# Kernel tuning notes

Hardware: AMD Instinct MI355X
Metric: run time of the kernel (lower is better)

## Reference

```python
import jax, jax.numpy as jnp
import numpy as np

D_MODEL = 1024
N_HEADS = 16
D_HEAD = D_MODEL // N_HEADS


def setup_inputs() -> dict:
    key = jax.random.key(0)
    k1, k2, k3 = jax.random.split(key, 3)
    B, T = 2, 2048
    x = jax.random.normal(k1, (B, T, D_MODEL), dtype=jnp.float32)
    # kaiming_normal fan_out on torch Linear weight [out, in]: std = sqrt(2/out)
    qkv_w = jax.random.normal(k2, (3 * D_MODEL, D_MODEL), dtype=jnp.float32) * np.sqrt(2.0 / (3 * D_MODEL)).astype(np.float32)
    out_w = jax.random.normal(k3, (D_MODEL, D_MODEL), dtype=jnp.float32) * np.sqrt(2.0 / D_MODEL).astype(np.float32)
    return {"x": x, "qkv_w": qkv_w, "out_w": out_w}


def rotate_half(x):
    x1, x2 = x[..., : x.shape[-1] // 2], x[..., x.shape[-1] // 2 :]
    return jnp.concatenate((-x2, x1), axis=-1)


def reference(x, qkv_w, out_w):
    B, T, D = x.shape
    H, dh = N_HEADS, D_HEAD
    scale = dh ** -0.5

    qkv = jnp.einsum('btd,ed->bte', x, qkv_w)  # [B,T,3D]
    q, k, v = jnp.split(qkv, 3, axis=-1)
    # [B,H,T,dh]
    q = q.reshape(B, T, H, dh).transpose(0, 2, 1, 3)
    k = k.reshape(B, T, H, dh).transpose(0, 2, 1, 3)
    v = v.reshape(B, T, H, dh).transpose(0, 2, 1, 3)

    # rotary embeddings
    inv_freq = 1.0 / (10000.0 ** (jnp.arange(0, dh, 2, dtype=jnp.float32) / dh))
    t = jnp.arange(T, dtype=jnp.float32)
    freqs = jnp.einsum('i,j->ij', t, inv_freq)        # [T, dh/2]
    emb = jnp.concatenate((freqs, freqs), axis=-1)    # [T, dh]
    cos = jnp.cos(emb)[None, None]                    # [1,1,T,dh]
    sin = jnp.sin(emb)[None, None]
    q = q * cos + rotate_half(q) * sin
    k = k * cos + rotate_half(k) * sin

    scores = jnp.einsum('bhqd,bhkd->bhqk', q, k) * scale
    causal = jnp.tril(jnp.ones((T, T), dtype=bool))
    scores = jnp.where(causal, scores, -jnp.inf)
    attn = jax.nn.softmax(scores, axis=-1)
    out = jnp.einsum('bhqk,bhkd->bhqd', attn, v)      # [B,H,T,dh]
    out = out.transpose(0, 2, 1, 3).reshape(B, T, D)
    return jnp.einsum('btd,ed->bte', out, out_w)
```

## Files before the change

### kernel.cpp

```cpp
#include <hip/hip_runtime.h>
#include <hip/hip_bf16.h>
#include <cmath>

#define Bb   2
#define Tseq 2048
#define NH   16
#define DM   1024

using f32x4 = __attribute__((ext_vector_type(4))) float;
using s16x8 = __attribute__((ext_vector_type(8))) short;
using s16x4 = __attribute__((ext_vector_type(4))) short;

typedef const __attribute__((address_space(1))) unsigned char* as1p;
typedef __attribute__((address_space(3))) unsigned char* as3p;

static __device__ __forceinline__ void gload_lds16(const void* g, void* l){
  __builtin_amdgcn_global_load_lds((as1p)g, (as3p)l, 16, 0, 0);
}

#if defined(__has_builtin)
#if __has_builtin(__builtin_amdgcn_mfma_f32_16x16x16bf16_1k)
#define MFMA16(acc, va, pb) (acc) = __builtin_amdgcn_mfma_f32_16x16x16bf16_1k((va), (pb), (acc), 0, 0, 0)
#endif
#endif
#ifndef MFMA16
#define MFMA16(acc, va, pb) asm volatile("s_nop 1\n\tv_mfma_f32_16x16x16_bf16 %0, %1, %2, %0" : "+v"(acc) : "v"(va), "v"(pb))
#endif

static __device__ __forceinline__ float b2f(unsigned short u){
  union { unsigned int u; float f; } v; v.u = ((unsigned int)u) << 16; return v.f;
}
static __device__ __forceinline__ unsigned short f2b(float f){
  union { float f; unsigned int u; } v; v.f = f;
  unsigned int u = v.u;
  return (unsigned short)((u + 0x7fffu + ((u >> 16) & 1u)) >> 16);
}

__global__ void k_convert(const float* __restrict__ in, unsigned short* __restrict__ out, int n){
  int stride = gridDim.x * blockDim.x;
  for (int i = blockIdx.x * blockDim.x + threadIdx.x; i * 4 < n; i += stride) {
    const float4 v = *reinterpret_cast<const float4*>(in + (size_t)i * 4);
    ushort4 o; o.x = f2b(v.x); o.y = f2b(v.y); o.z = f2b(v.z); o.w = f2b(v.w);
    *reinterpret_cast<ushort4*>(out + (size_t)i * 4) = o;
  }
}

template<int MODE>
__global__ __launch_bounds__(256) void k_gemm_bt(const unsigned short* __restrict__ A,
                                                 const unsigned short* __restrict__ W,
                                                 void* __restrict__ Cout,
                                                 int M, int N, int K, int NYL,
                                                 unsigned short* __restrict__ qr,
                                                 unsigned short* __restrict__ kr){
  __shared__ unsigned short As[128*64];
  __shared__ unsigned short Bs[128*64];
  const int i = (int)blockIdx.x;
  const int xcd = i & 7, rr = i >> 3;
  const int bx = rr / NYL, by = xcd * NYL + (rr % NYL);
  const int bm = bx * 128, bn = by * 128;
  const int tid = threadIdx.x;
  const int lane = tid & 63, w = tid >> 6;
  const int wr = w >> 1, wc = w & 1;
  const int g = lane >> 4, ln = lane & 15;
  f32x4 acc[4][4] = {};
  char* asb = (char*)As + w * 4096;
  char* bsb = (char*)Bs + w * 4096;
  const int lrow8 = lane >> 3;
  const int kcolb = ((lane & 7) ^ lrow8) * 16;
  const size_t aro = (size_t)(bm + w * 32 + lrow8) * K;
  const size_t bro = (size_t)(bn + w * 32 + lrow8) * K;
  const int xr = (ln & 7) << 4;
  for (int k0 = 0; k0 < K; k0 += 64) {
    #pragma unroll
    for (int q4 = 0; q4 < 4; ++q4) {
      gload_lds16((const char*)(A + aro + (size_t)(q4 * 8) * K + k0) + kcolb, asb + q4 * 1024);
      gload_lds16((const char*)(W + bro + (size_t)(q4 * 8) * K + k0) + kcolb, bsb + q4 * 1024);
    }
    __syncthreads();
    #pragma unroll
    for (int kk = 0; kk < 2; ++kk) {
      s16x8 af[4], bfr[4];
      const int ro = (kk * 64 + g * 16) ^ xr;
      #pragma unroll
      for (int mt = 0; mt < 4; ++mt)
        af[mt] = *reinterpret_cast<const s16x8*>((char*)As + (wr*64 + mt*16 + ln) * 128 + ro);
      #pragma unroll
      for (int nt = 0; nt < 4; ++nt)
        bfr[nt] = *reinterpret_cast<const s16x8*>((char*)Bs + (wc*64 + nt*16 + ln) * 128 + ro);
      #pragma unroll
      for (int mt = 0; mt < 4; ++mt)
        #pragma unroll
        for (int nt = 0; nt < 4; ++nt)
          acc[mt][nt] = __builtin_amdgcn_mfma_f32_16x16x32_bf16(af[mt], bfr[nt], acc[mt][nt], 0, 0, 0);
    }
    __syncthreads();
  }
  if (MODE == 0) {
    #pragma unroll
    for (int mt = 0; mt < 4; ++mt)
      #pragma unroll
      for (int nt = 0; nt < 4; ++nt)
        #pragma unroll
        for (int r = 0; r < 4; ++r) {
          int row = bm + wr*64 + mt*16 + g*4 + r;
          int col = bn + wc*64 + nt*16 + ln;
          reinterpret_cast<float*>(Cout)[(size_t)row * N + col] = acc[mt][nt][r];
        }
  } else {
    const int region = bn >> 10;
    if (region == 2) {
      #pragma unroll
      for (int mt = 0; mt < 4; ++mt)
        #pragma unroll
        for (int nt = 0; nt < 4; ++nt)
          #pragma unroll
          for (int r = 0; r < 4; ++r) {
            int row = bm + wr*64 + mt*16 + g*4 + r;
            int col = bn + wc*64 + nt*16 + ln;
            reinterpret_cast<unsigned short*>(Cout)[(size_t)row * N + col] = f2b(acc[mt][nt][r]);
          }
    } else {
      const float if0 = exp2f(-(float)ln        * 0.4152410118074f);
      const float if1 = exp2f(-(float)(16 + ln) * 0.4152410118074f);
      const int h = ((bn + wc * 64) >> 6) & 15;
      unsigned short* dst = (region == 0) ? qr : kr;
      const float qs = (region == 0) ? 0.18033688011112042f : 1.0f;
      #pragma unroll
      for (int mt = 0; mt < 4; ++mt)
        #pragma unroll
        for (int r = 0; r < 4; ++r) {
          int row = bm + wr*64 + mt*16 + g*4 + r;
          int t = row & (Tseq - 1), b = row >> 11;
          float c0, s0, c1, s1;
          __sincosf((float)t * if0, &s0, &c0);
          __sincosf((float)t * if1, &s1, &c1);
          float v0 = (acc[mt][0][r] * c0 - acc[mt][2][r] * s0) * qs;
          float v1 = (acc[mt][1][r] * c1 - acc[mt][3][r] * s1) * qs;
          float v2 = (acc[mt][2][r] * c0 + acc[mt][0][r] * s0) * qs;
          float v3 = (acc[mt][3][r] * c1 + acc[mt][1][r] * s1) * qs;
          size_t base = ((size_t)(b * NH + h) * Tseq + t) * 64 + ln;
          dst[base]      = f2b(v0);
          dst[base + 16] = f2b(v1);
          dst[base + 32] = f2b(v2);
          dst[base + 48] = f2b(v3);
        }
    }
  }
}

__global__ __launch_bounds__(256) void k_vtrans(const unsigned short* __restrict__ qkv,
                                                unsigned short* __restrict__ vt){
  __shared__ unsigned short L[64*72];
  const int blk = blockIdx.x;
  const int tt64 = blk & 31, bh = blk >> 5;
  const int b = bh >> 4, h = bh & 15;
  const int t0 = tt64 * 64;
  const int tid = threadIdx.x;
  {
    const int tr = tid >> 2, c = tid & 3;
    const unsigned short* src = qkv + ((size_t)(b * Tseq) + t0 + tr) * 3072 + 2048 + h * 64 + c * 16;
    uint4 a0 = *reinterpret_cast<const uint4*>(src);
    uint4 a1 = *reinterpret_cast<const uint4*>(src + 8);
    *reinterpret_cast<uint4*>(&L[tr * 72 + c * 16])     = a0;
    *reinterpret_cast<uint4*>(&L[tr * 72 + c * 16 + 8]) = a1;
  }
  __syncthreads();
  {
    const int d = tid >> 2, c = tid & 3;
    unsigned int wq[8];
    #pragma unroll
    for (int j = 0; j < 8; ++j) {
      unsigned int lo = L[(c * 16 + 2 * j)     * 72 + d];
      unsigned int hi = L[(c * 16 + 2 * j + 1) * 72 + d];
      wq[j] = lo | (hi << 16);
    }
    unsigned short* dst = vt + ((size_t)bh * 64 + d) * Tseq + t0 + c * 16;
    *reinterpret_cast<uint4*>(dst)     = make_uint4(wq[0], wq[1], wq[2], wq[3]);
    *reinterpret_cast<uint4*>(dst + 8) = make_uint4(wq[4], wq[5], wq[6], wq[7]);
  }
}

__global__ __launch_bounds__(256, 2) void k_attn(const unsigned short* __restrict__ Qr,
                                                 const unsigned short* __restrict__ Kr,
                                                 const unsigned short* __restrict__ Vt,
                                                 unsigned short* __restrict__ Ao){
  __shared__ unsigned short Ks[2][64*64];
  __shared__ unsigned short Vs[2][64*64];
  __shared__ unsigned short Ps[4][16*72];
  const int i = (int)blockIdx.x;
  const int xcd = i & 7, r = i >> 3;
  const int bh = xcd * 4 + (r >> 4);
  const int pj = r & 15;
  const unsigned short* Q  = Qr + (size_t)bh * Tseq * 64;
  const unsigned short* Kp = Kr + (size_t)bh * Tseq * 64;
  const unsigned short* Vp = Vt + (size_t)bh * 64 * Tseq;
  const int tid = threadIdx.x;
  const int w = tid >> 6, lane = tid & 63;
  const int g = lane >> 4, ln = lane & 15;
  const int srow = tid >> 2;
  const int c2 = (tid & 3) * 2;
  const int scol = c2 * 8;
  const int swz = (srow & 7) << 4;
  const int wb0 = srow * 128 + ((c2 * 16)      ^ swz);
  const int wb1 = srow * 128 + ((c2 * 16 + 16) ^ swz);
  const int x0 = (g * 16)      ^ ((ln & 7) << 4);
  const int x1 = (64 + g * 16) ^ ((ln & 7) << 4);
  unsigned short* Pw = Ps[w];
  const int b = bh / NH, h = bh % NH;

  #pragma unroll
  for (int pass = 0; pass < 2; ++pass) {
    const int j = pass ? (31 - pj) : pj;
    const int q0 = j * 64;
    const int ntiles = j + 1;
    const int q0w = q0 + w * 16;

    s16x8 qf0 = *reinterpret_cast<const s16x8*>(&Q[(size_t)(q0w + ln) * 64 + g * 8]);
    s16x8 qf1 = *reinterpret_cast<const s16x8*>(&Q[(size_t)(q0w + ln) * 64 + 32 + g * 8]);

    f32x4 oacc[4] = {};
    float lsum = 0.f;

    {
      const unsigned short* gk = Kp + (size_t)srow * 64 + scol;
      const unsigned short* gv = Vp + (size_t)srow * Tseq + scol;
      uint4 k0 = *reinterpret_cast<const uint4*>(gk);
      uint4 k1 = *reinterpret_cast<const uint4*>(gk + 8);
      uint4 v0 = *reinterpret_cast<const uint4*>(gv);
      uint4 v1 = *reinterpret_cast<const uint4*>(gv + 8);
      *reinterpret_cast<uint4*>((char*)Ks[0] + wb0) = k0;
      *reinterpret_cast<uint4*>((char*)Ks[0] + wb1) = k1;
      *reinterpret_cast<uint4*>((char*)Vs[0] + wb0) = v0;
      *reinterpret_cast<uint4*>((char*)Vs[0] + wb1) = v1;
    }
    __syncthreads();
    int cur = 0;

    for (int kt = 0; kt < ntiles; ++kt) {
      const bool pre = (kt + 1 < ntiles);
      const int nxt = cur ^ 1;
      uint4 nk0, nk1, nv0, nv1;
      if (pre) {
        const unsigned short* gk = Kp + (size_t)((kt + 1) * 64 + srow) * 64 + scol;
        const unsigned short* gv = Vp + (size_t)srow * Tseq + (kt + 1) * 64 + scol;
        nk0 = *reinterpret_cast<const uint4*>(gk);
        nk1 = *reinterpret_cast<const uint4*>(gk + 8);
        nv0 = *reinterpret_cast<const uint4*>(gv);
        nv1 = *reinterpret_cast<const uint4*>(gv + 8);
      }
      f32x4 s[4] = {};
      const char* kb = (const char*)Ks[cur];
      __builtin_amdgcn_s_setprio(1);
      #pragma unroll
      for (int nt = 0; nt < 4; ++nt) {
        s16x8 kfa = *reinterpret_cast<const s16x8*>(kb + nt * 2048 + ln * 128 + x0);
        s16x8 kfb = *reinterpret_cast<const s16x8*>(kb + nt * 2048 + ln * 128 + x1);
        s[nt] = __builtin_amdgcn_mfma_f32_16x16x32_bf16(kfa, qf0, s[nt], 0, 0, 0);
        s[nt] = __builtin_amdgcn_mfma_f32_16x16x32_bf16(kfb, qf1, s[nt], 0, 0, 0);
      }
      __builtin_amdgcn_s_setprio(0);
      if (kt == ntiles - 1) {
        #pragma unroll
        for (int nt = 0; nt < 4; ++nt)
          #pragma unroll
          for (int r2 = 0; r2 < 4; ++r2)
            if (nt * 16 + g * 4 + r2 > w * 16 + ln) s[nt][r2] = -1e30f;
      }
      s16x4 pb[4];
      #pragma unroll
      for (int nt = 0; nt < 4; ++nt)
        #pragma unroll
        for (int r2 = 0; r2 < 4; ++r2) {
          float p = __builtin_amdgcn_exp2f(s[nt][r2]);
          lsum += p;
          pb[nt][r2] = (short)(__float_as_uint(p) >> 16);
        }
      const char* vb = (const char*)Vs[cur];
      __builtin_amdgcn_s_setprio(1);
      #pragma unroll
      for (int dt = 0; dt < 4; ++dt) {
        #pragma unroll
        for (int nt = 0; nt < 4; ++nt) {
          s16x4 va = *reinterpret_cast<const s16x4*>(vb + (dt * 16 + ln) * 128 + ((nt * 32 + g * 8) ^ ((ln & 7) << 4)));
          MFMA16(oacc[dt], va, pb[nt]);
        }
      }
      __builtin_amdgcn_s_setprio(0);
      if (pre) {
        *reinterpret_cast<uint4*>((char*)Ks[nxt] + wb0) = nk0;
        *reinterpret_cast<uint4*>((char*)Ks[nxt] + wb1) = nk1;
        *reinterpret_cast<uint4*>((char*)Vs[nxt] + wb0) = nv0;
        *reinterpret_cast<uint4*>((char*)Vs[nxt] + wb1) = nv1;
      }
      __syncthreads();
      cur ^= 1;
    }

    float l = lsum;
    l += __shfl_xor(l, 16);
    l += __shfl_xor(l, 32);
    float inv = 1.f / l;
    #pragma unroll
    for (int nt = 0; nt < 4; ++nt) {
      unsigned int lo = (unsigned int)f2b(oacc[nt][0] * inv) | ((unsigned int)f2b(oacc[nt][1] * inv) << 16);
      unsigned int hi = (unsigned int)f2b(oacc[nt][2] * inv) | ((unsigned int)f2b(oacc[nt][3] * inv) << 16);
      *reinterpret_cast<uint2*>(&Pw[ln * 72 + nt * 16 + g * 4]) = make_uint2(lo, hi);
    }
    asm volatile("s_waitcnt lgkmcnt(0)" ::: "memory");
    __builtin_amdgcn_sched_barrier(0);
    const int rr = lane >> 2;
    const int cc = (lane & 3) * 8;
    uint4 ov0 = *reinterpret_cast<const uint4*>(&Pw[rr * 72 + cc]);
    uint4 ov1 = *reinterpret_cast<const uint4*>(&Pw[rr * 72 + cc + 32]);
    int t = q0w + rr;
    unsigned short* orow = &Ao[((size_t)(b * Tseq + t) * DM) + h * 64];
    *reinterpret_cast<uint4*>(orow + cc)      = ov0;
    *reinterpret_cast<uint4*>(orow + cc + 32) = ov1;
  }
}

extern "C" void kernel_launch(void* const* d_in, const int* in_sizes, int n_in,
                              void* d_out, int out_size, void* d_ws, size_t ws_size,
                              hipStream_t stream) {
  const float* x    = (const float*)d_in[0];
  const float* qkvw = (const float*)d_in[1];
  const float* outw = (const float*)d_in[2];
  float* out = (float*)d_out;
  char* ws = (char*)d_ws;
  size_t off = 0;
  auto alloc = [&](size_t bytes)->void*{ void* p = ws + off; off += (bytes + 255) & ~(size_t)255; return p; };
  unsigned short* x_bf   = (unsigned short*)alloc((size_t)Bb*Tseq*DM*2);
  unsigned short* qw_bf  = (unsigned short*)alloc((size_t)3*DM*DM*2);
  unsigned short* ow_bf  = (unsigned short*)alloc((size_t)DM*DM*2);
  unsigned short* qkv_bf = (unsigned short*)alloc((size_t)Bb*Tseq*3*DM*2);
  unsigned short* qr     = (unsigned short*)alloc((size_t)Bb*NH*Tseq*64*2);
  unsigned short* kr     = (unsigned short*)alloc((size_t)Bb*NH*Tseq*64*2);
  unsigned short* vt     = (unsigned short*)alloc((size_t)Bb*NH*Tseq*64*2);
  unsigned short* ao     = (unsigned short*)alloc((size_t)Bb*Tseq*DM*2);
  (void)ws_size; (void)in_sizes; (void)n_in; (void)out_size;

  const int nx  = Bb*Tseq*DM;
  const int nqw = 3*DM*DM;
  const int now = DM*DM;
  k_convert<<<2048, 256, 0, stream>>>(x, x_bf, nx);
  k_convert<<<2048, 256, 0, stream>>>(qkvw, qw_bf, nqw);
  k_convert<<<1024, 256, 0, stream>>>(outw, ow_bf, now);
  k_gemm_bt<2><<<768, 256, 0, stream>>>(x_bf, qw_bf, qkv_bf, Bb*Tseq, 3*DM, DM, 3, qr, kr);
  k_vtrans<<<Bb*NH*(Tseq/64), 256, 0, stream>>>(qkv_bf, vt);
  k_attn<<<dim3(Bb*NH*16), 256, 0, stream>>>(qr, kr, vt, ao);
  k_gemm_bt<0><<<256, 256, 0, stream>>>(ao, ow_bf, out, Bb*Tseq, DM, DM, 1, qr, kr);
}
```

Before: 114.5 us.

## Fuse V transpose into QKV GEMM, merge converts, one query tile per attention block

Merges the three fp32-to-bf16 conversion launches into one kernel. The QKV GEMM now transposes the V tile through shared memory in its epilogue and writes Vt directly, which removes the intermediate qkv buffer and the separate transpose kernel. Attention now gives each block a single query tile, scheduled longest-first across twice as many blocks, and raises the occupancy hint from 2 to 5. The output staging reuses the K shared buffer, so the load balance across blocks changes and register pressure rises under the tighter launch bound.

Measured after the change: 123.7 us. +8.0%, slower.

```diff
diff --git a/kernel.cpp b/kernel.cpp
--- a/kernel.cpp
+++ b/kernel.cpp
@@ -36,12 +36,19 @@
   return (unsigned short)((u + 0x7fffu + ((u >> 16) & 1u)) >> 16);
 }
 
-__global__ void k_convert(const float* __restrict__ in, unsigned short* __restrict__ out, int n){
-  int stride = gridDim.x * blockDim.x;
-  for (int i = blockIdx.x * blockDim.x + threadIdx.x; i * 4 < n; i += stride) {
-    const float4 v = *reinterpret_cast<const float4*>(in + (size_t)i * 4);
+__global__ void k_convert3(const float* __restrict__ a, unsigned short* __restrict__ ab, int na,
+                           const float* __restrict__ b, unsigned short* __restrict__ bb, int nb,
+                           const float* __restrict__ c, unsigned short* __restrict__ cb, int nc){
+  const int q0 = na >> 2, q1 = nb >> 2, q2 = nc >> 2;
+  const int tot = q0 + q1 + q2;
+  const int stride = gridDim.x * blockDim.x;
+  for (int i = blockIdx.x * blockDim.x + threadIdx.x; i < tot; i += stride) {
+    const float* src; unsigned short* dst; int j = i;
+    if (j < q0) { src = a; dst = ab; }
+    else { j -= q0; if (j < q1) { src = b; dst = bb; } else { j -= q1; src = c; dst = cb; } }
+    float4 v = reinterpret_cast<const float4*>(src)[j];
     ushort4 o; o.x = f2b(v.x); o.y = f2b(v.y); o.z = f2b(v.z); o.w = f2b(v.w);
-    *reinterpret_cast<ushort4*>(out + (size_t)i * 4) = o;
+    reinterpret_cast<ushort4*>(dst)[j] = o;
   }
 }
 
@@ -51,7 +58,8 @@
                                                  void* __restrict__ Cout,
                                                  int M, int N, int K, int NYL,
                                                  unsigned short* __restrict__ qr,
-                                                 unsigned short* __restrict__ kr){
+                                                 unsigned short* __restrict__ kr,
+                                                 unsigned short* __restrict__ vt){
   __shared__ unsigned short As[128*64];
   __shared__ unsigned short Bs[128*64];
   const int i = (int)blockIdx.x;
@@ -109,16 +117,42 @@
   } else {
     const int region = bn >> 10;
     if (region == 2) {
-      #pragma unroll
-      for (int mt = 0; mt < 4; ++mt)
-        #pragma unroll
-        for (int nt = 0; nt < 4; ++nt)
-          #pragma unroll
-          for (int r = 0; r < 4; ++r) {
-            int row = bm + wr*64 + mt*16 + g*4 + r;
-            int col = bn + wc*64 + nt*16 + ln;
-            reinterpret_cast<unsigned short*>(Cout)[(size_t)row * N + col] = f2b(acc[mt][nt][r]);
-          }
+      unsigned short* tb = wc ? Bs : As;
+      #pragma unroll
+      for (int nt = 0; nt < 4; ++nt) {
+        const int lrow = nt * 16 + ln;
+        char* rowp = (char*)tb + lrow * 256;
+        const int sx = (lrow & 15) << 3;
+        #pragma unroll
+        for (int mt = 0; mt < 4; ++mt) {
+          const int t2 = (wr*64 + mt*16 + g*4) * 2;
+          unsigned int lo = (unsigned int)f2b(acc[mt][nt][0]) | ((unsigned int)f2b(acc[mt][nt][1]) << 16);
+          unsigned int hi = (unsigned int)f2b(acc[mt][nt][2]) | ((unsigned int)f2b(acc[mt][nt][3]) << 16);
+          *reinterpret_cast<uint2*>(rowp + (t2 ^ sx)) = make_uint2(lo, hi);
+        }
+      }
+      __syncthreads();
+      {
+        const int dcol = tid >> 1, half = tid & 1;
+        unsigned short* tb2 = (dcol < 64) ? As : Bs;
+        char* rowp = (char*)tb2 + (dcol & 63) * 256;
+        const int sx = (dcol & 15) << 3;
+        unsigned int buf[32];
+        #pragma unroll
+        for (int k = 0; k < 16; ++k) {
+          uint2 v = *reinterpret_cast<uint2*>(rowp + ((((half * 64 + k * 4) * 2) ^ sx)));
+          buf[k*2] = v.x; buf[k*2+1] = v.y;
+        }
+        const int h0 = (bn - 2048) >> 6;
+        const int hq = h0 + (dcol >> 6);
+        const int dd = dcol & 63;
+        const int row0 = bm + half * 64;
+        const int b = row0 >> 11, t0 = row0 & (Tseq - 1);
+        unsigned short* dst = vt + ((size_t)((b * NH + hq) * 64 + dd)) * Tseq + t0;
+        #pragma unroll
+        for (int k = 0; k < 8; ++k)
+          reinterpret_cast<uint4*>(dst)[k] = make_uint4(buf[k*4], buf[k*4+1], buf[k*4+2], buf[k*4+3]);
+      }
     } else {
       const float if0 = exp2f(-(float)ln        * 0.4152410118074f);
       const float if1 = exp2f(-(float)(16 + ln) * 0.4152410118074f);
@@ -148,49 +182,18 @@
   }
 }
 
-__global__ __launch_bounds__(256) void k_vtrans(const unsigned short* __restrict__ qkv,
-                                                unsigned short* __restrict__ vt){
-  __shared__ unsigned short L[64*72];
-  const int blk = blockIdx.x;
-  const int tt64 = blk & 31, bh = blk >> 5;
-  const int b = bh >> 4, h = bh & 15;
-  const int t0 = tt64 * 64;
-  const int tid = threadIdx.x;
-  {
-    const int tr = tid >> 2, c = tid & 3;
-    const unsigned short* src = qkv + ((size_t)(b * Tseq) + t0 + tr) * 3072 + 2048 + h * 64 + c * 16;
-    uint4 a0 = *reinterpret_cast<const uint4*>(src);
-    uint4 a1 = *reinterpret_cast<const uint4*>(src + 8);
-    *reinterpret_cast<uint4*>(&L[tr * 72 + c * 16])     = a0;
-    *reinterpret_cast<uint4*>(&L[tr * 72 + c * 16 + 8]) = a1;
-  }
-  __syncthreads();
-  {
-    const int d = tid >> 2, c = tid & 3;
-    unsigned int wq[8];
-    #pragma unroll
-    for (int j = 0; j < 8; ++j) {
-      unsigned int lo = L[(c * 16 + 2 * j)     * 72 + d];
-      unsigned int hi = L[(c * 16 + 2 * j + 1) * 72 + d];
-      wq[j] = lo | (hi << 16);
-    }
-    unsigned short* dst = vt + ((size_t)bh * 64 + d) * Tseq + t0 + c * 16;
-    *reinterpret_cast<uint4*>(dst)     = make_uint4(wq[0], wq[1], wq[2], wq[3]);
-    *reinterpret_cast<uint4*>(dst + 8) = make_uint4(wq[4], wq[5], wq[6], wq[7]);
-  }
-}
-
-__global__ __launch_bounds__(256, 2) void k_attn(const unsigned short* __restrict__ Qr,
+__global__ __launch_bounds__(256, 5) void k_attn(const unsigned short* __restrict__ Qr,
                                                  const unsigned short* __restrict__ Kr,
                                                  const unsigned short* __restrict__ Vt,
                                                  unsigned short* __restrict__ Ao){
   __shared__ unsigned short Ks[2][64*64];
   __shared__ unsigned short Vs[2][64*64];
-  __shared__ unsigned short Ps[4][16*72];
   const int i = (int)blockIdx.x;
   const int xcd = i & 7, r = i >> 3;
-  const int bh = xcd * 4 + (r >> 4);
-  const int pj = r & 15;
+  const int qt = 31 - (r >> 2);
+  const int bh = xcd * 4 + (r & 3);
+  const int q0 = qt * 64;
+  const int ntiles = qt + 1;
   const unsigned short* Q  = Qr + (size_t)bh * Tseq * 64;
   const unsigned short* Kp = Kr + (size_t)bh * Tseq * 64;
   const unsigned short* Vp = Vt + (size_t)bh * 64 * Tseq;
@@ -205,118 +208,111 @@
   const int wb1 = srow * 128 + ((c2 * 16 + 16) ^ swz);
   const int x0 = (g * 16)      ^ ((ln & 7) << 4);
   const int x1 = (64 + g * 16) ^ ((ln & 7) << 4);
-  unsigned short* Pw = Ps[w];
   const int b = bh / NH, h = bh % NH;
-
+  const int q0w = q0 + w * 16;
+
+  s16x8 qf0 = *reinterpret_cast<const s16x8*>(&Q[(size_t)(q0w + ln) * 64 + g * 8]);
+  s16x8 qf1 = *reinterpret_cast<const s16x8*>(&Q[(size_t)(q0w + ln) * 64 + 32 + g * 8]);
+
+  f32x4 oacc[4] = {};
+  float lsum = 0.f;
+
+  {
+    const unsigned short* gk = Kp + (size_t)srow * 64 + scol;
+    const unsigned short* gv = Vp + (size_t)srow * Tseq + scol;
+    uint4 k0 = *reinterpret_cast<const uint4*>(gk);
+    uint4 k1 = *reinterpret_cast<const uint4*>(gk + 8);
+    uint4 v0 = *reinterpret_cast<const uint4*>(gv);
+    uint4 v1 = *reinterpret_cast<const uint4*>(gv + 8);
+    *reinterpret_cast<uint4*>((char*)Ks[0] + wb0) = k0;
+    *reinterpret_cast<uint4*>((char*)Ks[0] + wb1) = k1;
+    *reinterpret_cast<uint4*>((char*)Vs[0] + wb0) = v0;
+    *reinterpret_cast<uint4*>((char*)Vs[0] + wb1) = v1;
+  }
+  __syncthreads();
+  int cur = 0;
+
+  for (int kt = 0; kt < ntiles; ++kt) {
+    const bool pre = (kt + 1 < ntiles);
+    const int nxt = cur ^ 1;
+    uint4 nk0, nk1, nv0, nv1;
+    if (pre) {
+      const unsigned short* gk = Kp + (size_t)((kt + 1) * 64 + srow) * 64 + scol;
+      const unsigned short* gv = Vp + (size_t)srow * Tseq + (kt + 1) * 64 + scol;
+      nk0 = *reinterpret_cast<const uint4*>(gk);
+      nk1 = *reinterpret_cast<const uint4*>(gk + 8);
+      nv0 = *reinterpret_cast<const uint4*>(gv);
+      nv1 = *reinterpret_cast<const uint4*>(gv + 8);
+    }
+    f32x4 s[4] = {};
+    const char* kb = (const char*)Ks[cur];
+    __builtin_amdgcn_s_setprio(1);
+    #pragma unroll
+    for (int nt = 0; nt < 4; ++nt) {
+      s16x8 kfa = *reinterpret_cast<const s16x8*>(kb + nt * 2048 + ln * 128 + x0);
+      s16x8 kfb = *reinterpret_cast<const s16x8*>(kb + nt * 2048 + ln * 128 + x1);
+      s[nt] = __builtin_amdgcn_mfma_f32_16x16x32_bf16(kfa, qf0, s[nt], 0, 0, 0);
+      s[nt] = __builtin_amdgcn_mfma_f32_16x16x32_bf16(kfb, qf1, s[nt], 0, 0, 0);
+    }
+    __builtin_amdgcn_s_setprio(0);
+    if (kt == ntiles - 1) {
+      #pragma unroll
+      for (int nt = 0; nt < 4; ++nt)
+        #pragma unroll
+        for (int r2 = 0; r2 < 4; ++r2)
+          if (nt * 16 + g * 4 + r2 > w * 16 + ln) s[nt][r2] = -1e30f;
+    }
+    s16x4 pb[4];
+    #pragma unroll
+    for (int nt = 0; nt < 4; ++nt)
+      #pragma unroll
+      for (int r2 = 0; r2 < 4; ++r2) {
+        float p = __builtin_amdgcn_exp2f(s[nt][r2]);
+        lsum += p;
+        pb[nt][r2] = (short)(__float_as_uint(p) >> 16);
+      }
+    const char* vb = (const char*)Vs[cur];
+    __builtin_amdgcn_s_setprio(1);
+    #pragma unroll
+    for (int dt = 0; dt < 4; ++dt) {
+      #pragma unroll
+      for (int nt = 0; nt < 4; ++nt) {
+        s16x4 va = *reinterpret_cast<const s16x4*>(vb + (dt * 16 + ln) * 128 + ((nt * 32 + g * 8) ^ ((ln & 7) << 4)));
+        MFMA16(oacc[dt], va, pb[nt]);
+      }
+    }
+    __builtin_amdgcn_s_setprio(0);
+    if (pre) {
+      *reinterpret_cast<uint4*>((char*)Ks[nxt] + wb0) = nk0;
+      *reinterpret_cast<uint4*>((char*)Ks[nxt] + wb1) = nk1;
+      *reinterpret_cast<uint4*>((char*)Vs[nxt] + wb0) = nv0;
+      *reinterpret_cast<uint4*>((char*)Vs[nxt] + wb1) = nv1;
+    }
+    __syncthreads();
+    cur ^= 1;
+  }
+
+  float l = lsum;
+  l += __shfl_xor(l, 16);
+  l += __shfl_xor(l, 32);
+  float inv = 1.f / l;
+  unsigned short* Pw = reinterpret_cast<unsigned short*>((char*)Ks + w * 4096);
   #pragma unroll
-  for (int pass = 0; pass < 2; ++pass) {
-    const int j = pass ? (31 - pj) : pj;
-    const int q0 = j * 64;
-    const int ntiles = j + 1;
-    const int q0w = q0 + w * 16;
-
-    s16x8 qf0 = *reinterpret_cast<const s16x8*>(&Q[(size_t)(q0w + ln) * 64 + g * 8]);
-    s16x8 qf1 = *reinterpret_cast<const s16x8*>(&Q[(size_t)(q0w + ln) * 64 + 32 + g * 8]);
-
-    f32x4 oacc[4] = {};
-    float lsum = 0.f;
-
-    {
-      const unsigned short* gk = Kp + (size_t)srow * 64 + scol;
-      const unsigned short* gv = Vp + (size_t)srow * Tseq + scol;
-      uint4 k0 = *reinterpret_cast<const uint4*>(gk);
-      uint4 k1 = *reinterpret_cast<const uint4*>(gk + 8);
-      uint4 v0 = *reinterpret_cast<const uint4*>(gv);
-      uint4 v1 = *reinterpret_cast<const uint4*>(gv + 8);
-      *reinterpret_cast<uint4*>((char*)Ks[0] + wb0) = k0;
-      *reinterpret_cast<uint4*>((char*)Ks[0] + wb1) = k1;
-      *reinterpret_cast<uint4*>((char*)Vs[0] + wb0) = v0;
-      *reinterpret_cast<uint4*>((char*)Vs[0] + wb1) = v1;
-    }
-    __syncthreads();
-    int cur = 0;
-
-    for (int kt = 0; kt < ntiles; ++kt) {
-      const bool pre = (kt + 1 < ntiles);
-      const int nxt = cur ^ 1;
-      uint4 nk0, nk1, nv0, nv1;
-      if (pre) {
-        const unsigned short* gk = Kp + (size_t)((kt + 1) * 64 + srow) * 64 + scol;
-        const unsigned short* gv = Vp + (size_t)srow * Tseq + (kt + 1) * 64 + scol;
-        nk0 = *reinterpret_cast<const uint4*>(gk);
-        nk1 = *reinterpret_cast<const uint4*>(gk + 8);
-        nv0 = *reinterpret_cast<const uint4*>(gv);
-        nv1 = *reinterpret_cast<const uint4*>(gv + 8);
-      }
-      f32x4 s[4] = {};
-      const char* kb = (const char*)Ks[cur];
-      __builtin_amdgcn_s_setprio(1);
-      #pragma unroll
-      for (int nt = 0; nt < 4; ++nt) {
-        s16x8 kfa = *reinterpret_cast<const s16x8*>(kb + nt * 2048 + ln * 128 + x0);
-        s16x8 kfb = *reinterpret_cast<const s16x8*>(kb + nt * 2048 + ln * 128 + x1);
-        s[nt] = __builtin_amdgcn_mfma_f32_16x16x32_bf16(kfa, qf0, s[nt], 0, 0, 0);
-        s[nt] = __builtin_amdgcn_mfma_f32_16x16x32_bf16(kfb, qf1, s[nt], 0, 0, 0);
-      }
-      __builtin_amdgcn_s_setprio(0);
-      if (kt == ntiles - 1) {
-        #pragma unroll
-        for (int nt = 0; nt < 4; ++nt)
-          #pragma unroll
-          for (int r2 = 0; r2 < 4; ++r2)
-            if (nt * 16 + g * 4 + r2 > w * 16 + ln) s[nt][r2] = -1e30f;
-      }
-      s16x4 pb[4];
-      #pragma unroll
-      for (int nt = 0; nt < 4; ++nt)
-        #pragma unroll
-        for (int r2 = 0; r2 < 4; ++r2) {
-          float p = __builtin_amdgcn_exp2f(s[nt][r2]);
-          lsum += p;
-          pb[nt][r2] = (short)(__float_as_uint(p) >> 16);
-        }
-      const char* vb = (const char*)Vs[cur];
-      __builtin_amdgcn_s_setprio(1);
-      #pragma unroll
-      for (int dt = 0; dt < 4; ++dt) {
-        #pragma unroll
-        for (int nt = 0; nt < 4; ++nt) {
-          s16x4 va = *reinterpret_cast<const s16x4*>(vb + (dt * 16 + ln) * 128 + ((nt * 32 + g * 8) ^ ((ln & 7) << 4)));
-          MFMA16(oacc[dt], va, pb[nt]);
-        }
-      }
-      __builtin_amdgcn_s_setprio(0);
-      if (pre) {
-        *reinterpret_cast<uint4*>((char*)Ks[nxt] + wb0) = nk0;
-        *reinterpret_cast<uint4*>((char*)Ks[nxt] + wb1) = nk1;
-        *reinterpret_cast<uint4*>((char*)Vs[nxt] + wb0) = nv0;
-        *reinterpret_cast<uint4*>((char*)Vs[nxt] + wb1) = nv1;
-      }
-      __syncthreads();
-      cur ^= 1;
-    }
-
-    float l = lsum;
-    l += __shfl_xor(l, 16);
-    l += __shfl_xor(l, 32);
-    float inv = 1.f / l;
-    #pragma unroll
-    for (int nt = 0; nt < 4; ++nt) {
-      unsigned int lo = (unsigned int)f2b(oacc[nt][0] * inv) | ((unsigned int)f2b(oacc[nt][1] * inv) << 16);
-      unsigned int hi = (unsigned int)f2b(oacc[nt][2] * inv) | ((unsigned int)f2b(oacc[nt][3] * inv) << 16);
-      *reinterpret_cast<uint2*>(&Pw[ln * 72 + nt * 16 + g * 4]) = make_uint2(lo, hi);
-    }
-    asm volatile("s_waitcnt lgkmcnt(0)" ::: "memory");
-    __builtin_amdgcn_sched_barrier(0);
-    const int rr = lane >> 2;
-    const int cc = (lane & 3) * 8;
-    uint4 ov0 = *reinterpret_cast<const uint4*>(&Pw[rr * 72 + cc]);
-    uint4 ov1 = *reinterpret_cast<const uint4*>(&Pw[rr * 72 + cc + 32]);
-    int t = q0w + rr;
-    unsigned short* orow = &Ao[((size_t)(b * Tseq + t) * DM) + h * 64];
-    *reinterpret_cast<uint4*>(orow + cc)      = ov0;
-    *reinterpret_cast<uint4*>(orow + cc + 32) = ov1;
-  }
+  for (int nt = 0; nt < 4; ++nt) {
+    unsigned int lo = (unsigned int)f2b(oacc[nt][0] * inv) | ((unsigned int)f2b(oacc[nt][1] * inv) << 16);
+    unsigned int hi = (unsigned int)f2b(oacc[nt][2] * inv) | ((unsigned int)f2b(oacc[nt][3] * inv) << 16);
+    *reinterpret_cast<uint2*>(&Pw[ln * 72 + nt * 16 + g * 4]) = make_uint2(lo, hi);
+  }
+  asm volatile("s_waitcnt lgkmcnt(0)" ::: "memory");
+  __builtin_amdgcn_sched_barrier(0);
+  const int rr2 = lane >> 2;
+  const int cc = (lane & 3) * 8;
+  uint4 ov0 = *reinterpret_cast<const uint4*>(&Pw[rr2 * 72 + cc]);
+  uint4 ov1 = *reinterpret_cast<const uint4*>(&Pw[rr2 * 72 + cc + 32]);
+  int t = q0w + rr2;
+  unsigned short* orow = &Ao[((size_t)(b * Tseq + t) * DM) + h * 64];
+  *reinterpret_cast<uint4*>(orow + cc)      = ov0;
+  *reinterpret_cast<uint4*>(orow + cc + 32) = ov1;
 }
 
 extern "C" void kernel_launch(void* const* d_in, const int* in_sizes, int n_in,
@@ -332,7 +328,6 @@
   unsigned short* x_bf   = (unsigned short*)alloc((size_t)Bb*Tseq*DM*2);
   unsigned short* qw_bf  = (unsigned short*)alloc((size_t)3*DM*DM*2);
   unsigned short* ow_bf  = (unsigned short*)alloc((size_t)DM*DM*2);
-  unsigned short* qkv_bf = (unsigned short*)alloc((size_t)Bb*Tseq*3*DM*2);
   unsigned short* qr     = (unsigned short*)alloc((size_t)Bb*NH*Tseq*64*2);
   unsigned short* kr     = (unsigned short*)alloc((size_t)Bb*NH*Tseq*64*2);
   unsigned short* vt     = (unsigned short*)alloc((size_t)Bb*NH*Tseq*64*2);
@@ -342,11 +337,8 @@
   const int nx  = Bb*Tseq*DM;
   const int nqw = 3*DM*DM;
   const int now = DM*DM;
-  k_convert<<<2048, 256, 0, stream>>>(x, x_bf, nx);
-  k_convert<<<2048, 256, 0, stream>>>(qkvw, qw_bf, nqw);
-  k_convert<<<1024, 256, 0, stream>>>(outw, ow_bf, now);
-  k_gemm_bt<2><<<768, 256, 0, stream>>>(x_bf, qw_bf, qkv_bf, Bb*Tseq, 3*DM, DM, 3, qr, kr);
-  k_vtrans<<<Bb*NH*(Tseq/64), 256, 0, stream>>>(qkv_bf, vt);
-  k_attn<<<dim3(Bb*NH*16), 256, 0, stream>>>(qr, kr, vt, ao);
-  k_gemm_bt<0><<<256, 256, 0, stream>>>(ao, ow_bf, out, Bb*Tseq, DM, DM, 1, qr, kr);
-}
+  k_convert3<<<2048, 256, 0, stream>>>(x, x_bf, nx, qkvw, qw_bf, nqw, outw, ow_bf, now);
+  k_gemm_bt<2><<<768, 256, 0, stream>>>(x_bf, qw_bf, nullptr, Bb*Tseq, 3*DM, DM, 3, qr, kr, vt);
+  k_attn<<<dim3(Bb*NH*32), 256, 0, stream>>>(qr, kr, vt, ao);
+  k_gemm_bt<0><<<256, 256, 0, stream>>>(ao, ow_bf, out, Bb*Tseq, DM, DM, 1, qr, kr, vt);
+}
```
